# Performance work log

Measured on AMD Instinct MI355X. Metric: run time of the kernel, lower is better.

Reference implementation:

```python
import jax, jax.numpy as jnp
import numpy as np

N, E, G = 50000, 800000, 128          # nodes, edges, graphs in batch
DF, DE, DT = 128, 256, 18             # dim_features, dim_embedding, dim_target
NUM_LAYERS = 4


def setup_inputs() -> dict:
    key = jax.random.key(0)
    ks = jax.random.split(key, 32)
    inp = {}
    inp["x"] = jax.random.normal(ks[0], (N, DF), jnp.float32)
    inp["edge_index"] = jax.random.randint(ks[1], (2, E), 0, N, dtype=jnp.int64)
    inp["batch"] = jnp.sort(jax.random.randint(ks[2], (N,), 0, G, dtype=jnp.int64))
    i = 3
    for l in range(NUM_LAYERS):
        din = DF if l == 0 else DE
        inp[f"Wl{l}"] = jax.random.normal(ks[i], (din, DE), jnp.float32) * (din ** -0.5); i += 1
        inp[f"bl{l}"] = jnp.zeros((DE,), jnp.float32)
        inp[f"Wr{l}"] = jax.random.normal(ks[i], (din, DE), jnp.float32) * (din ** -0.5); i += 1
        inp[f"Wm{l}"] = jax.random.normal(ks[i], (DE, DE), jnp.float32) * (DE ** -0.5); i += 1
        inp[f"bm{l}"] = jnp.zeros((DE,), jnp.float32)
    inp["fc1_W"] = jax.random.normal(ks[i], (NUM_LAYERS * DE, DE), jnp.float32) * ((NUM_LAYERS * DE) ** -0.5); i += 1
    inp["fc1_b"] = jnp.zeros((DE,), jnp.float32)
    inp["fc2_W"] = jax.random.normal(ks[i], (DE, DT), jnp.float32) * (DE ** -0.5); i += 1
    inp["fc2_b"] = jnp.zeros((DT,), jnp.float32)
    return inp


def _seg_max(v, idx, n):
    # scatter-max; empty segments -> 0 (PyG scatter 'max' convention)
    m = jax.ops.segment_max(v, idx, num_segments=n)
    return jnp.where(jnp.isfinite(m), m, 0.0)


def reference(x, edge_index, batch,
              Wl0, bl0, Wr0, Wm0, bm0,
              Wl1, bl1, Wr1, Wm1, bm1,
              Wl2, bl2, Wr2, Wm2, bm2,
              Wl3, bl3, Wr3, Wm3, bm3,
              fc1_W, fc1_b, fc2_W, fc2_b):
    src, dst = edge_index[0], edge_index[1]
    params = [(Wl0, bl0, Wr0, Wm0, bm0), (Wl1, bl1, Wr1, Wm1, bm1),
              (Wl2, bl2, Wr2, Wm2, bm2), (Wl3, bl3, Wr3, Wm3, bm3)]
    h = x
    outs = []
    for Wl, bl, Wr, Wm, bm in params:
        # SAGEConv(aggr='max'): lin_l(max_j x_j) + lin_r(x_i)
        agg = _seg_max(h[src], dst, h.shape[0])       # [N, din] gather + scatter-max
        h = agg @ Wl + bl + h @ Wr                    # [N, DE]
        h = jax.nn.relu(h @ Wm + bm)                  # fc_max + relu
        outs.append(h)
    hc = jnp.concatenate(outs, axis=1)                # [N, 4*DE]
    g = _seg_max(hc, batch, G)                        # global_max_pool -> [G, 4*DE]
    last_layer = jax.nn.relu(g @ fc1_W + fc1_b)       # [G, DE]
    out = last_layer @ fc2_W + fc2_b                  # [G, DT] (dropout = identity at eval)
    return jax.nn.log_softmax(out, axis=1), out, last_layer
```

## Files before the change

### kernel.cpp

```cpp
#include <hip/hip_runtime.h>
#include <stdint.h>

#define NN 50000
#define EE 800000
#define GG 128
#define DF 128
#define DE 256
#define NB 196

typedef unsigned short u16;
typedef __bf16 bf16x8 __attribute__((ext_vector_type(8)));
typedef float f32x4 __attribute__((ext_vector_type(4)));
typedef short s16x8 __attribute__((ext_vector_type(8)));

__device__ __forceinline__ float bf2f(u16 u) {
  union { unsigned int i; float f; } x; x.i = ((unsigned int)u) << 16; return x.f;
}
__device__ __forceinline__ u16 f2bf(float f) {
  union { float f; unsigned int i; } x; x.f = f;
  unsigned int i = x.i;
  return (u16)((i + 0x7fffu + ((i >> 16) & 1u)) >> 16);
}

__device__ __forceinline__ void async16(const void* g, void* l) {
  __builtin_amdgcn_global_load_lds(
      (const __attribute__((address_space(1))) void*)g,
      (__attribute__((address_space(3))) void*)l,
      16, 0, 0);
}

__device__ __forceinline__ s16x8 vmax8(s16x8 a, s16x8 b) {
  return __builtin_elementwise_max(a, b);
}

__global__ void detect_kernel(const u16* __restrict__ xr,
                              const unsigned* __restrict__ ei_words,
                              int* __restrict__ flags, int* __restrict__ bucket_cnt) {
  int tid = threadIdx.x;
  if (blockIdx.x == 1) {
    if (tid < NB) bucket_cnt[tid] = 0;
    return;
  }
  __shared__ int red[2];
  if (tid < 2) red[tid] = 0;
  __syncthreads();
  int found = 0;
  for (int it = 0; it < 32; it++) {
    int i = it * 256 + tid;
    u16 a = xr[2 * i], b = xr[2 * i + 1];
    if (((a >> 7) & 0xFFu) == 0xFFu) found = 1;
    if (((b >> 7) & 0xFFu) == 0xFFu) found = 1;
  }
  if (__ballot(found)) { if ((tid & 63) == 0) atomicOr(&red[0], 1); }
  int nz = 0;
  if (tid < 128) {
    for (int j = 0; j < 4; j++) {
      unsigned w = ei_words[2 * (tid * 4 + j) + 1];
      if (w != 0u) nz = 1;
    }
  }
  if (__ballot(nz)) { if ((tid & 63) == 0) atomicOr(&red[1], 1); }
  __syncthreads();
  if (tid == 0) { flags[0] = red[0]; flags[1] = red[1]; }
}

__device__ __forceinline__ u16 ldw(const void* p, int idx, int f) {
  return f ? f2bf(((const float*)p)[idx]) : ((const u16*)p)[idx];
}

struct ConvSeg { const void* src; u16* dst; int start_blk; int n; };

struct PrepArgs {
  ConvSeg s[12]; int nseg; int conv_blocks;
  const void* x; u16* acat_x; u16* xk;
  const void* ei; const void* batch;
  int* src32; int* dst32; int* batch32; int* bucket_cnt;
};

__global__ void prep_all(PrepArgs A, const int* __restrict__ flags) {
  int f = flags[0];
  int tid = threadIdx.x;
  int b = blockIdx.x;

  if (b < A.conv_blocks) {
    for (int i = 0; i < A.nseg; i++) {
      int nb = (A.s[i].n + 255) >> 8;
      if (b >= A.s[i].start_blk && b < A.s[i].start_blk + nb) {
        int idx = ((b - A.s[i].start_blk) << 8) + tid;
        if (idx < A.s[i].n) A.s[i].dst[idx] = ldw(A.s[i].src, idx, f);
        return;
      }
    }
    return;
  }
  b -= A.conv_blocks;

  if (b < 3125) {
    int i = (b * 256 + tid) * 8;
    int node = i >> 7, d = i & 127;
    union { u16 u[8]; uint4 v; } o, kx;
    if (f) {
      const float4* xp = (const float4*)((const float*)A.x + i);
      float4 a = xp[0], q = xp[1];
      o.u[0] = f2bf(a.x); o.u[1] = f2bf(a.y); o.u[2] = f2bf(a.z); o.u[3] = f2bf(a.w);
      o.u[4] = f2bf(q.x); o.u[5] = f2bf(q.y); o.u[6] = f2bf(q.z); o.u[7] = f2bf(q.w);
    } else {
      o.v = *(const uint4*)((const u16*)A.x + i);
    }
#pragma unroll
    for (int j = 0; j < 8; j++) {
      short s = (short)o.u[j];
      kx.u[j] = (u16)(s ^ ((s >> 15) & 0x7FFF));
    }
    *(uint4*)(A.acat_x + (long)node * 512 + d) = o.v;
    *(uint4*)(A.xk + i) = kx.v;
    return;
  }
  b -= 3125;

  __shared__ int h[NB];
  if (tid < NB) h[tid] = 0;
  __syncthreads();
  int i64 = (flags[1] == 0);
  int e0 = b * 2048;
  for (int j = 0; j < 8; j++) {
    int i = e0 + j * 256 + tid;
    if (i < EE) {
      int s, d;
      if (i64) {
        s = (int)((const long long*)A.ei)[i];
        d = (int)((const long long*)A.ei)[EE + i];
      } else {
        s = ((const int*)A.ei)[i];
        d = ((const int*)A.ei)[EE + i];
      }
      s = min(max(s, 0), NN - 1);
      d = min(max(d, 0), NN - 1);
      A.src32[i] = s;
      A.dst32[i] = d;
      atomicAdd(&h[d >> 8], 1);
    }
    if (i < NN) {
      int bv = i64 ? (int)((const long long*)A.batch)[i] : ((const int*)A.batch)[i];
      A.batch32[i] = min(max(bv, 0), GG - 1);
    }
  }
  __syncthreads();
  if (tid < NB) atomicAdd(&A.bucket_cnt[tid], h[tid]);
}

struct TransArgs {
  const void* Wl[4]; const void* Wr[4]; const void* Wm[4]; const void* fc1W;
  u16* WcatT[4]; u16* WmT[4]; u16* fc1WT;
};

__global__ __launch_bounds__(256) void transpose_w(TransArgs T, const int* __restrict__ flags) {
  int f = flags[0];
  __shared__ u16 tile[64][65];
  int b = blockIdx.x;
  const void* src; u16* dst; int kt, ntile, Kd; int krow_off = 0;
  if (b < 16) {
    kt = b >> 2; ntile = b & 3; Kd = 256;
    if (kt * 64 < 128) { src = T.Wl[0]; } else { src = T.Wr[0]; krow_off = 128; }
    dst = T.WcatT[0];
  } else if (b < 112) {
    int l = 1 + (b - 16) / 32; int t = (b - 16) % 32;
    kt = t >> 2; ntile = t & 3; Kd = 512;
    if (kt * 64 < 256) { src = T.Wl[l]; } else { src = T.Wr[l]; krow_off = 256; }
    dst = T.WcatT[l];
  } else if (b < 176) {
    int l = (b - 112) / 16; int t = (b - 112) % 16;
    kt = t >> 2; ntile = t & 3; Kd = 256;
    src = T.Wm[l]; dst = T.WmT[l];
  } else {
    int t = b - 176;
    kt = t >> 2; ntile = t & 3; Kd = 1024;
    src = T.fc1W; dst = T.fc1WT;
  }
  int cj = threadIdx.x & 63, rp = threadIdx.x >> 6;
#pragma unroll 4
  for (int p = 0; p < 16; p++) {
    int krow = kt * 64 + p * 4 + rp;
    tile[p * 4 + rp][cj] = ldw(src, (krow - krow_off) * 256 + ntile * 64 + cj, f);
  }
  __syncthreads();
#pragma unroll 4
  for (int p = 0; p < 16; p++) {
    int nrow = ntile * 64 + p * 4 + rp;
    dst[(long)nrow * Kd + kt * 64 + cj] = tile[cj][p * 4 + rp];
  }
}

__global__ void bucket_scan(const int* __restrict__ bucket_cnt, int* __restrict__ bucket_base,
                            int* __restrict__ bucket_cur,
                            const int* __restrict__ batch, int* __restrict__ gs) {
  __shared__ int sh[256];
  int tid = threadIdx.x;
  int x = (tid < NB) ? bucket_cnt[tid] : 0;
  sh[tid] = x;
  __syncthreads();
  for (int off = 1; off < 256; off <<= 1) {
    int v = (tid >= off) ? sh[tid - off] : 0;
    __syncthreads();
    sh[tid] += v;
    __syncthreads();
  }
  if (tid < NB) { bucket_base[tid] = sh[tid] - x; bucket_cur[tid] = sh[tid] - x; }
  if (tid == 0) bucket_base[NB] = EE;
  if (tid <= GG) {
    int g = tid, lo = 0, hi = NN;
    while (lo < hi) { int mid = (lo + hi) >> 1; if (batch[mid] < g) lo = mid + 1; else hi = mid; }
    gs[g] = lo;
  }
}

__global__ __launch_bounds__(256) void bucket_pass1(
    const int* __restrict__ src32, const int* __restrict__ dst32,
    int* __restrict__ bucket_cur, unsigned* __restrict__ bucket_buf) {
  __shared__ int lcnt[NB];
  __shared__ int lbase[NB];
  int tid = threadIdx.x, b = blockIdx.x;
  if (tid < NB) lcnt[tid] = 0;
  __syncthreads();
  int e0 = b * 2048;
  int lofs[8]; unsigned pk[8]; int bk[8];
#pragma unroll
  for (int j = 0; j < 8; j++) {
    int i = e0 + j * 256 + tid;
    if (i < EE) {
      int s = src32[i], d = dst32[i];
      bk[j] = d >> 8;
      pk[j] = ((unsigned)s << 8) | (unsigned)(d & 255);
      lofs[j] = atomicAdd(&lcnt[bk[j]], 1);
    } else bk[j] = -1;
  }
  __syncthreads();
  if (tid < NB) lbase[tid] = atomicAdd(&bucket_cur[tid], lcnt[tid]);
  __syncthreads();
#pragma unroll
  for (int j = 0; j < 8; j++)
    if (bk[j] >= 0)
      bucket_buf[lbase[bk[j]] + lofs[j]] = pk[j];
}

__global__ __launch_bounds__(256) void bucket_pass2(
    const unsigned* __restrict__ bucket_buf, const int* __restrict__ bucket_base,
    int* __restrict__ col_src, int* __restrict__ row_ptr) {
  __shared__ int cnt[256];
  __shared__ int sh[256];
  __shared__ int cur[256];
  int tid = threadIdx.x, b = blockIdx.x;
  int ebase = bucket_base[b], eend = bucket_base[b + 1];
  cnt[tid] = 0;
  __syncthreads();
  for (int e = ebase + tid; e < eend; e += 256)
    atomicAdd(&cnt[bucket_buf[e] & 255u], 1);
  __syncthreads();
  int x = cnt[tid];
  sh[tid] = x;
  __syncthreads();
  for (int off = 1; off < 256; off <<= 1) {
    int v = (tid >= off) ? sh[tid - off] : 0;
    __syncthreads();
    sh[tid] += v;
    __syncthreads();
  }
  int node = b * 256 + tid;
  if (node < NN) row_ptr[node + 1] = ebase + sh[tid];
  cur[tid] = ebase + sh[tid] - x;
  __syncthreads();
  for (int e = ebase + tid; e < eend; e += 256) {
    unsigned p = bucket_buf[e];
    int slot = atomicAdd(&cur[p & 255u], 1);
    col_src[slot] = (int)(p >> 8);
  }
  if (b == 0 && tid == 0) row_ptr[0] = 0;
}

template <int LPR, bool KEYED>
__global__ __launch_bounds__(256) void segmax_kernel(
    const u16* __restrict__ feat, int fstride,
    const int* __restrict__ row_ptr, const int* __restrict__ col_src,
    u16* __restrict__ agg_out, int ostride, int n) {
  constexpr int R = 64 / LPR;
  int node = blockIdx.x * 4 + (threadIdx.x >> 6);
  if (node >= n) return;
  int lane = threadIdx.x & 63;
  int sub = lane / LPR;
  int cp = lane % LPR;
  int beg = row_ptr[node], end = row_ptr[node + 1];
  s16x8 m = (s16x8)(short)(KEYED ? (short)0x807F : (short)0);
  const u16* fb = feat + cp * 8;

  int e = beg + sub;
  for (; e + 3 * R < end; e += 4 * R) {
    int s0 = col_src[e];
    int s1 = col_src[e + R];
    int s2 = col_src[e + 2 * R];
    int s3 = col_src[e + 3 * R];
    s16x8 v0 = *(const s16x8*)(fb + (long)s0 * fstride);
    s16x8 v1 = *(const s16x8*)(fb + (long)s1 * fstride);
    s16x8 v2 = *(const s16x8*)(fb + (long)s2 * fstride);
    s16x8 v3 = *(const s16x8*)(fb + (long)s3 * fstride);
    m = vmax8(m, vmax8(vmax8(v0, v1), vmax8(v2, v3)));
  }
  for (; e < end; e += R)
    m = vmax8(m, *(const s16x8*)(fb + (long)col_src[e] * fstride));

#pragma unroll
  for (int d = LPR; d < 64; d <<= 1) {
    union { s16x8 s; int i[4]; } t;
    t.s = m;
#pragma unroll
    for (int j = 0; j < 4; j++) t.i[j] = __shfl_xor(t.i[j], d);
    m = vmax8(m, t.s);
  }

  if (sub == 0) {
    if (KEYED) {
      if (beg == end) {
        m = (s16x8)(short)0;
      } else {
        s16x8 sp = (m >> 15) & (short)0x7FFF;
        m = m ^ sp;
      }
    }
    *(s16x8*)(agg_out + (long)node * ostride + cp * 8) = m;
  }
}

__global__ __launch_bounds__(512) void gemm256w(
    const u16* __restrict__ A, int lda, int K,
    const u16* __restrict__ BT,
    const u16* __restrict__ bias,
    u16* __restrict__ C, int ldc, int M, int relu_flag) {
  __shared__ u16 lsA[128 * 64];
  __shared__ u16 lsB[256 * 64];
  int tid = threadIdx.x;
  int lane = tid & 63, w = tid >> 6;
  int bm = blockIdx.x;
  int wm = (w & 1) << 6, wn = (w >> 1) << 6;
  int ln15 = lane & 15, quad = lane >> 4;

  f32x4 acc[4][4] = {};

  int riw = lane >> 3;
  int j = (lane & 7) ^ riw;
  int ra0 = min(bm * 128 + w * 8 + riw, M - 1);
  int ra1 = min(bm * 128 + 64 + w * 8 + riw, M - 1);
  const u16* gA0 = A + (long)ra0 * lda + j * 8;
  const u16* gA1 = A + (long)ra1 * lda + j * 8;
  const u16* gB0 = BT + (long)(w * 8 + riw) * K + j * 8;
  const u16* gB1 = BT + (long)(64 + w * 8 + riw) * K + j * 8;
  const u16* gB2 = BT + (long)(128 + w * 8 + riw) * K + j * 8;
  const u16* gB3 = BT + (long)(192 + w * 8 + riw) * K + j * 8;
  u16* lA0 = lsA + (w * 8) * 64;
  u16* lA1 = lsA + (64 + w * 8) * 64;
  u16* lB0 = lsB + (w * 8) * 64;
  u16* lB1 = lsB + (64 + w * 8) * 64;
  u16* lB2 = lsB + (128 + w * 8) * 64;
  u16* lB3 = lsB + (192 + w * 8) * 64;
  int swz7 = ln15 & 7;

  for (int k0 = 0; k0 < K; k0 += 64) {
    async16(gA0 + k0, lA0);
    async16(gA1 + k0, lA1);
    async16(gB0 + k0, lB0);
    async16(gB1 + k0, lB1);
    async16(gB2 + k0, lB2);
    async16(gB3 + k0, lB3);
    __syncthreads();
#pragma unroll
    for (int kh = 0; kh < 2; kh++) {
      int pc = (((kh << 2) | quad) ^ swz7) << 3;
      bf16x8 af[4], bfr[4];
#pragma unroll
      for (int t = 0; t < 4; t++) {
        af[t]  = *(const bf16x8*)(lsA + (wm + t * 16 + ln15) * 64 + pc);
        bfr[t] = *(const bf16x8*)(lsB + (wn + t * 16 + ln15) * 64 + pc);
      }
#pragma unroll
      for (int mt = 0; mt < 4; mt++)
#pragma unroll
        for (int nt = 0; nt < 4; nt++)
          acc[mt][nt] = __builtin_amdgcn_mfma_f32_16x16x32_bf16(af[mt], bfr[nt], acc[mt][nt], 0, 0, 0);
    }
    __syncthreads();
  }

  float bv[4];
#pragma unroll
  for (int nt = 0; nt < 4; nt++)
    bv[nt] = bf2f(bias[wn + nt * 16 + ln15]);

#pragma unroll
  for (int mt = 0; mt < 4; mt++) {
    int row0 = bm * 128 + wm + mt * 16 + quad * 4;
#pragma unroll
    for (int rr = 0; rr < 4; rr++) {
      int row = row0 + rr;
      if (row < M) {
#pragma unroll
        for (int nt = 0; nt < 4; nt++) {
          float v = acc[mt][nt][rr] + bv[nt];
          if (relu_flag) v = fmaxf(v, 0.f);
          C[(long)row * ldc + wn + nt * 16 + ln15] = f2bf(v);
        }
      }
    }
  }
}

__global__ void pool_kernel(const u16* __restrict__ h, const int* __restrict__ gs,
                            u16* __restrict__ g_pool, int l) {
  int g = blockIdx.x >> 1, half = blockIdx.x & 1;
  int chunk = threadIdx.x & 15;
  int rg = threadIdx.x >> 4;
  int beg = gs[g], end = gs[g + 1];
  s16x8 m = (s16x8)(short)0;
  const u16* hp = h + half * 128 + chunk * 8;
  for (int n = beg + rg; n < end; n += 64)
    m = vmax8(m, *(const s16x8*)(hp + (long)n * 512));
  __shared__ s16x8 red[64][16];
  red[rg][chunk] = m;
  __syncthreads();
  for (int s = 32; s >= 1; s >>= 1) {
    if (rg < s) red[rg][chunk] = vmax8(red[rg][chunk], red[rg + s][chunk]);
    __syncthreads();
  }
  if (rg == 0)
    *(s16x8*)(g_pool + g * 1024 + l * 256 + half * 128 + chunk * 8) = red[0][chunk];
}

__global__ __launch_bounds__(256) void fc1_gemm(
    const u16* __restrict__ A,
    const u16* __restrict__ BT,
    float* __restrict__ Cpart) {
  __shared__ u16 lsA[128 * 32];
  __shared__ u16 lsB[128 * 32];
  int tid = threadIdx.x;
  int lane = tid & 63, w = tid >> 6;
  int slice = blockIdx.x >> 1, bn = blockIdx.x & 1;
  int wm = (w & 1) << 6, wn = (w >> 1) << 6;
  int ln15 = lane & 15, quad = lane >> 4;

  f32x4 acc[4][4] = {};

  int cm = lane >> 2;
  int ck = (lane & 3) << 3;
  int kb = slice * 256;

  const u16* gA0 = A + (long)(w * 16 + cm) * 1024 + kb + ck;
  const u16* gA1 = A + (long)((w + 4) * 16 + cm) * 1024 + kb + ck;
  const u16* gB0 = BT + (long)(bn * 128 + w * 16 + cm) * 1024 + kb + ck;
  const u16* gB1 = BT + (long)(bn * 128 + (w + 4) * 16 + cm) * 1024 + kb + ck;
  u16* lA0 = lsA + w * 512;
  u16* lA1 = lsA + (w + 4) * 512;
  u16* lB0 = lsB + w * 512;
  u16* lB1 = lsB + (w + 4) * 512;

  for (int k0 = 0; k0 < 256; k0 += 32) {
    async16(gA0 + k0, lA0);
    async16(gA1 + k0, lA1);
    async16(gB0 + k0, lB0);
    async16(gB1 + k0, lB1);
    __syncthreads();
    bf16x8 af[4], bfr[4];
#pragma unroll
    for (int t = 0; t < 4; t++) {
      af[t]  = *(const bf16x8*)(lsA + (wm + t * 16 + ln15) * 32 + quad * 8);
      bfr[t] = *(const bf16x8*)(lsB + (wn + t * 16 + ln15) * 32 + quad * 8);
    }
#pragma unroll
    for (int mt = 0; mt < 4; mt++)
#pragma unroll
      for (int nt = 0; nt < 4; nt++)
        acc[mt][nt] = __builtin_amdgcn_mfma_f32_16x16x32_bf16(af[mt], bfr[nt], acc[mt][nt], 0, 0, 0);
    __syncthreads();
  }

  float* Cb = Cpart + slice * (GG * 256);
#pragma unroll
  for (int mt = 0; mt < 4; mt++) {
    int row0 = wm + mt * 16 + quad * 4;
#pragma unroll
    for (int r = 0; r < 4; r++)
#pragma unroll
      for (int nt = 0; nt < 4; nt++)
        Cb[(row0 + r) * 256 + bn * 128 + wn + nt * 16 + ln15] = acc[mt][nt][r];
  }
}

__global__ void fc2_head(const float* __restrict__ fc1part,
                         const u16* __restrict__ fc1b,
                         const u16* __restrict__ W,
                         const u16* __restrict__ b,
                         void* __restrict__ outbuf, const int* __restrict__ flags) {
  int g = blockIdx.x, t = threadIdx.x;
  __shared__ float lr[256];
  __shared__ float ps[144];
  __shared__ float sv[18];
  __shared__ float sred[2];
  float v = bf2f(fc1b[t]);
#pragma unroll
  for (int s = 0; s < 4; s++) v += fc1part[s * (GG * 256) + g * 256 + t];
  v = fmaxf(v, 0.f);
  lr[t] = v;
  if (flags[0]) ((float*)outbuf)[4608 + g * 256 + t] = v;
  else          ((u16*)outbuf)[4608 + g * 256 + t] = f2bf(v);
  __syncthreads();
  if (t < 144) {
    int o = t % 18, s = t / 18;
    float acc = 0.f;
    int k0 = s * 32;
#pragma unroll 8
    for (int k = k0; k < k0 + 32; k++)
      acc += lr[k] * bf2f(W[k * 18 + o]);
    ps[t] = acc;
  }
  __syncthreads();
  if (t < 18) {
    float acc = bf2f(b[t]);
#pragma unroll
    for (int s = 0; s < 8; s++) acc += ps[s * 18 + t];
    sv[t] = acc;
  }
  __syncthreads();
  if (t == 0) {
    float mx = sv[0];
    for (int i = 1; i < 18; i++) mx = fmaxf(mx, sv[i]);
    float s = 0.f;
    for (int i = 0; i < 18; i++) s += expf(sv[i] - mx);
    sred[0] = mx; sred[1] = logf(s);
  }
  __syncthreads();
  if (t < 18) {
    float raw = sv[t];
    float lsm = raw - sred[0] - sred[1];
    if (flags[0]) {
      ((float*)outbuf)[g * 18 + t] = lsm;
      ((float*)outbuf)[2304 + g * 18 + t] = raw;
    } else {
      ((u16*)outbuf)[g * 18 + t] = f2bf(lsm);
      ((u16*)outbuf)[2304 + g * 18 + t] = f2bf(raw);
    }
  }
}

extern "C" void kernel_launch(void* const* d_in, const int* in_sizes, int n_in,
                              void* d_out, int out_size, void* d_ws, size_t ws_size,
                              hipStream_t stream) {
  (void)in_sizes; (void)n_in; (void)out_size; (void)ws_size;
  const void* x = d_in[0];
  const void* ei = d_in[1];
  const void* batch = d_in[2];
  const void *Wl[4], *bl[4], *Wr[4], *Wm[4], *bm[4];
  for (int l = 0; l < 4; l++) {
    Wl[l] = d_in[3 + l * 5 + 0];
    bl[l] = d_in[3 + l * 5 + 1];
    Wr[l] = d_in[3 + l * 5 + 2];
    Wm[l] = d_in[3 + l * 5 + 3];
    bm[l] = d_in[3 + l * 5 + 4];
  }
  const void* fc1W = d_in[23];
  const void* fc1b = d_in[24];
  const void* fc2W = d_in[25];
  const void* fc2b = d_in[26];

  char* ws = (char*)d_ws;
  size_t off = 0;
  auto alloc = [&](size_t bytes) -> void* {
    void* p = ws + off;
    off = (off + bytes + 255) & ~(size_t)255;
    return p;
  };
  int* flags       = (int*)alloc(16);
  int* row_ptr     = (int*)alloc((NN + 1) * sizeof(int));
  int* bucket_cnt  = (int*)alloc(NB * sizeof(int));
  int* bucket_base = (int*)alloc((NB + 1) * sizeof(int));
  int* bucket_cur  = (int*)alloc(NB * sizeof(int));
  unsigned* bucket_buf = (unsigned*)alloc((size_t)EE * sizeof(unsigned));
  int* col_src = (int*)alloc((size_t)EE * sizeof(int));
  int* src32   = (int*)alloc((size_t)EE * sizeof(int));
  int* dst32   = (int*)alloc((size_t)EE * sizeof(int));
  int* batch32 = (int*)alloc(NN * sizeof(int));
  int* gs      = (int*)alloc((GG + 1) * sizeof(int));
  u16* WcatT[4]; for (int l = 0; l < 4; l++) WcatT[l] = (u16*)alloc(256 * 512 * 2);
  u16* WmT[4];   for (int l = 0; l < 4; l++) WmT[l]   = (u16*)alloc(256 * 256 * 2);
  u16* bl_bf[4]; for (int l = 0; l < 4; l++) bl_bf[l] = (u16*)alloc(256 * 2);
  u16* bm_bf[4]; for (int l = 0; l < 4; l++) bm_bf[l] = (u16*)alloc(256 * 2);
  u16* fc1WT   = (u16*)alloc(256 * 1024 * 2);
  u16* fc1b_bf = (u16*)alloc(256 * 2);
  u16* fc2W_bf = (u16*)alloc(256 * 18 * 2);
  u16* fc2b_bf = (u16*)alloc(18 * 2);
  u16* xk      = (u16*)alloc((size_t)NN * DF * 2);
  u16* Acat    = (u16*)alloc((size_t)NN * 512 * 2);
  u16* tmp     = (u16*)alloc((size_t)NN * 256 * 2);
  u16* gpool   = (u16*)alloc(GG * 1024 * 2);
  float* fc1part = (float*)alloc(4 * GG * 256 * sizeof(float));

  detect_kernel<<<2, 256, 0, stream>>>((const u16*)x, (const unsigned*)ei, flags, bucket_cnt);

  TransArgs TA;
  for (int l = 0; l < 4; l++) {
    TA.Wl[l] = Wl[l]; TA.Wr[l] = Wr[l]; TA.Wm[l] = Wm[l];
    TA.WcatT[l] = WcatT[l]; TA.WmT[l] = WmT[l];
  }
  TA.fc1W = fc1W; TA.fc1WT = fc1WT;
  transpose_w<<<240, 256, 0, stream>>>(TA, flags);

  PrepArgs PA;
  int blk = 0, si = 0;
  auto addseg = [&](const void* s, u16* d, int n) {
    PA.s[si].src = s; PA.s[si].dst = d; PA.s[si].start_blk = blk; PA.s[si].n = n;
    blk += (n + 255) / 256; si++;
  };
  addseg(fc2W, fc2W_bf, 256 * 18);
  for (int l = 0; l < 4; l++) addseg(bl[l], bl_bf[l], 256);
  for (int l = 0; l < 4; l++) addseg(bm[l], bm_bf[l], 256);
  addseg(fc1b, fc1b_bf, 256);
  addseg(fc2b, fc2b_bf, 18);
  PA.nseg = si; PA.conv_blocks = blk;
  PA.x = x; PA.acat_x = Acat + DF; PA.xk = xk;
  PA.ei = ei; PA.batch = batch;
  PA.src32 = src32; PA.dst32 = dst32; PA.batch32 = batch32; PA.bucket_cnt = bucket_cnt;
  prep_all<<<PA.conv_blocks + 3125 + 391, 256, 0, stream>>>(PA, flags);

  bucket_scan<<<1, 256, 0, stream>>>(bucket_cnt, bucket_base, bucket_cur, batch32, gs);
  bucket_pass1<<<391, 256, 0, stream>>>(src32, dst32, bucket_cur, bucket_buf);
  bucket_pass2<<<NB, 256, 0, stream>>>(bucket_buf, bucket_base, col_src, row_ptr);

  int segblocks = (NN + 3) / 4;
  int gemmgrid = (NN + 127) / 128;

  for (int l = 0; l < 4; l++) {
    if (l == 0) {
      segmax_kernel<16, true><<<segblocks, 256, 0, stream>>>(xk, DF, row_ptr, col_src,
                                                             Acat, 512, NN);
    } else {
      segmax_kernel<32, false><<<segblocks, 256, 0, stream>>>(Acat + 256, 512, row_ptr, col_src,
                                                              Acat, 512, NN);
    }
    int K = (l == 0) ? 256 : 512;
    gemm256w<<<gemmgrid, 512, 0, stream>>>(Acat, 512, K, WcatT[l], bl_bf[l], tmp, 256, NN, 0);
    gemm256w<<<gemmgrid, 512, 0, stream>>>(tmp, 256, 256, WmT[l], bm_bf[l], Acat + 256, 512, NN, 1);
    pool_kernel<<<GG * 2, 1024, 0, stream>>>(Acat + 256, gs, gpool, l);
  }

  fc1_gemm<<<8, 256, 0, stream>>>(gpool, fc1WT, fc1part);
  fc2_head<<<GG, 256, 0, stream>>>(fc1part, fc1b_bf, fc2W_bf, fc2b_bf, d_out, flags);
}
```

Before: 535.5 us.

## Store node features in 32-column sliced layout for cache-friendly gather

Replaces the interleaved [N,512] concat buffer with a column-sliced layout: 16 planes of [N,32] bf16. Neighbour-max gathers now run per slice, so each gathered row is 64 contiguous bytes and the working set per block fits in cache. The GEMM A-load, GEMM epilogue, prep and pool kernels are updated to address the new layout. In exchange the segmax launches 8x more blocks, so row_ptr and col_src are read once per slice, and the C stores from the GEMM use a strided pattern.

```diff
diff --git a/kernel.cpp b/kernel.cpp
--- a/kernel.cpp
+++ b/kernel.cpp
@@ -7,6 +7,7 @@
 #define DF 128
 #define DE 256
 #define NB 196
+#define SLPITCH (NN * 32)
 
 typedef unsigned short u16;
 typedef __bf16 bf16x8 __attribute__((ext_vector_type(8)));
@@ -72,7 +73,7 @@
 
 struct PrepArgs {
   ConvSeg s[12]; int nseg; int conv_blocks;
-  const void* x; u16* acat_x; u16* xk;
+  const void* x; u16* Asl; u16* xk;
   const void* ei; const void* batch;
   int* src32; int* dst32; int* batch32; int* bucket_cnt;
 };
@@ -112,7 +113,7 @@
       short s = (short)o.u[j];
       kx.u[j] = (u16)(s ^ ((s >> 15) & 0x7FFF));
     }
-    *(uint4*)(A.acat_x + (long)node * 512 + d) = o.v;
+    *(uint4*)(A.Asl + (size_t)(4 + (d >> 5)) * SLPITCH + (long)node * 32 + (d & 31)) = o.v;
     *(uint4*)(A.xk + i) = kx.v;
     return;
   }
@@ -277,20 +278,19 @@
   if (b == 0 && tid == 0) row_ptr[0] = 0;
 }
 
-template <int LPR, bool KEYED>
-__global__ __launch_bounds__(256) void segmax_kernel(
-    const u16* __restrict__ feat, int fstride,
+__global__ __launch_bounds__(256) void segmax_l0(
+    const u16* __restrict__ xk,
     const int* __restrict__ row_ptr, const int* __restrict__ col_src,
-    u16* __restrict__ agg_out, int ostride, int n) {
-  constexpr int R = 64 / LPR;
+    u16* __restrict__ Asl, int n) {
+  constexpr int LPR = 16, R = 4;
   int node = blockIdx.x * 4 + (threadIdx.x >> 6);
   if (node >= n) return;
   int lane = threadIdx.x & 63;
   int sub = lane / LPR;
   int cp = lane % LPR;
   int beg = row_ptr[node], end = row_ptr[node + 1];
-  s16x8 m = (s16x8)(short)(KEYED ? (short)0x807F : (short)0);
-  const u16* fb = feat + cp * 8;
+  s16x8 m = (s16x8)(short)0x807F;
+  const u16* fb = xk + cp * 8;
 
   int e = beg + sub;
   for (; e + 3 * R < end; e += 4 * R) {
@@ -298,14 +298,14 @@
     int s1 = col_src[e + R];
     int s2 = col_src[e + 2 * R];
     int s3 = col_src[e + 3 * R];
-    s16x8 v0 = *(const s16x8*)(fb + (long)s0 * fstride);
-    s16x8 v1 = *(const s16x8*)(fb + (long)s1 * fstride);
-    s16x8 v2 = *(const s16x8*)(fb + (long)s2 * fstride);
-    s16x8 v3 = *(const s16x8*)(fb + (long)s3 * fstride);
+    s16x8 v0 = *(const s16x8*)(fb + (long)s0 * DF);
+    s16x8 v1 = *(const s16x8*)(fb + (long)s1 * DF);
+    s16x8 v2 = *(const s16x8*)(fb + (long)s2 * DF);
+    s16x8 v3 = *(const s16x8*)(fb + (long)s3 * DF);
     m = vmax8(m, vmax8(vmax8(v0, v1), vmax8(v2, v3)));
   }
   for (; e < end; e += R)
-    m = vmax8(m, *(const s16x8*)(fb + (long)col_src[e] * fstride));
+    m = vmax8(m, *(const s16x8*)(fb + (long)col_src[e] * DF));
 
 #pragma unroll
   for (int d = LPR; d < 64; d <<= 1) {
@@ -317,23 +317,59 @@
   }
 
   if (sub == 0) {
-    if (KEYED) {
-      if (beg == end) {
-        m = (s16x8)(short)0;
-      } else {
-        s16x8 sp = (m >> 15) & (short)0x7FFF;
-        m = m ^ sp;
-      }
-    }
-    *(s16x8*)(agg_out + (long)node * ostride + cp * 8) = m;
-  }
+    if (beg == end) {
+      m = (s16x8)(short)0;
+    } else {
+      s16x8 sp = (m >> 15) & (short)0x7FFF;
+      m = m ^ sp;
+    }
+    *(s16x8*)(Asl + (size_t)(cp >> 2) * SLPITCH + (long)node * 32 + (cp & 3) * 8) = m;
+  }
+}
+
+__global__ __launch_bounds__(256) void segmax_sl(
+    const u16* __restrict__ Asl,
+    const int* __restrict__ row_ptr, const int* __restrict__ col_src, int n) {
+  int s = blockIdx.x & 7;
+  int node = (blockIdx.x >> 3) * 4 + (threadIdx.x >> 6);
+  if (node >= n) return;
+  int lane = threadIdx.x & 63;
+  int sub = lane >> 2;
+  int cp = lane & 3;
+  int beg = row_ptr[node], end = row_ptr[node + 1];
+  s16x8 m = (s16x8)(short)0;
+  const u16* fb = Asl + (size_t)(8 + s) * SLPITCH + cp * 8;
+
+  int e = beg + sub;
+  for (; e + 16 < end; e += 32) {
+    int s0 = col_src[e];
+    int s1 = col_src[e + 16];
+    s16x8 v0 = *(const s16x8*)(fb + (long)s0 * 32);
+    s16x8 v1 = *(const s16x8*)(fb + (long)s1 * 32);
+    m = vmax8(m, vmax8(v0, v1));
+  }
+  if (e < end)
+    m = vmax8(m, *(const s16x8*)(fb + (long)col_src[e] * 32));
+
+#pragma unroll
+  for (int d = 4; d < 64; d <<= 1) {
+    union { s16x8 s; int i[4]; } t;
+    t.s = m;
+#pragma unroll
+    for (int j = 0; j < 4; j++) t.i[j] = __shfl_xor(t.i[j], d);
+    m = vmax8(m, t.s);
+  }
+
+  if (sub == 0)
+    *(s16x8*)((u16*)Asl + (size_t)s * SLPITCH + (long)node * 32 + cp * 8) = m;
 }
 
 __global__ __launch_bounds__(512) void gemm256w(
-    const u16* __restrict__ A, int lda, int K,
+    const u16* __restrict__ A, int lda, int K, int a_sliced,
     const u16* __restrict__ BT,
     const u16* __restrict__ bias,
-    u16* __restrict__ C, int ldc, int M, int relu_flag) {
+    u16* __restrict__ C, int ldc,
+    int M, int relu_flag, int c_sliced) {
   __shared__ u16 lsA[128 * 64];
   __shared__ u16 lsB[256 * 64];
   int tid = threadIdx.x;
@@ -348,8 +384,6 @@
   int j = (lane & 7) ^ riw;
   int ra0 = min(bm * 128 + w * 8 + riw, M - 1);
   int ra1 = min(bm * 128 + 64 + w * 8 + riw, M - 1);
-  const u16* gA0 = A + (long)ra0 * lda + j * 8;
-  const u16* gA1 = A + (long)ra1 * lda + j * 8;
   const u16* gB0 = BT + (long)(w * 8 + riw) * K + j * 8;
   const u16* gB1 = BT + (long)(64 + w * 8 + riw) * K + j * 8;
   const u16* gB2 = BT + (long)(128 + w * 8 + riw) * K + j * 8;
@@ -363,8 +397,18 @@
   int swz7 = ln15 & 7;
 
   for (int k0 = 0; k0 < K; k0 += 64) {
-    async16(gA0 + k0, lA0);
-    async16(gA1 + k0, lA1);
+    const u16 *pA0, *pA1;
+    if (a_sliced) {
+      int c = (k0 >> 3) + j;
+      size_t so = (size_t)(c >> 2) * SLPITCH + (c & 3) * 8;
+      pA0 = A + so + (long)ra0 * 32;
+      pA1 = A + so + (long)ra1 * 32;
+    } else {
+      pA0 = A + (long)ra0 * lda + k0 + j * 8;
+      pA1 = A + (long)ra1 * lda + k0 + j * 8;
+    }
+    async16(pA0, lA0);
+    async16(pA1, lA1);
     async16(gB0 + k0, lB0);
     async16(gB1 + k0, lB1);
     async16(gB2 + k0, lB2);
@@ -394,33 +438,44 @@
     bv[nt] = bf2f(bias[wn + nt * 16 + ln15]);
 
 #pragma unroll
-  for (int mt = 0; mt < 4; mt++) {
-    int row0 = bm * 128 + wm + mt * 16 + quad * 4;
-#pragma unroll
-    for (int rr = 0; rr < 4; rr++) {
-      int row = row0 + rr;
-      if (row < M) {
-#pragma unroll
-        for (int nt = 0; nt < 4; nt++) {
+  for (int nt = 0; nt < 4; nt++) {
+    int col = wn + nt * 16 + ln15;
+    u16* cb;
+    long rstride;
+    if (c_sliced) {
+      cb = C + (size_t)(8 + (col >> 5)) * SLPITCH + (col & 31);
+      rstride = 32;
+    } else {
+      cb = C + col;
+      rstride = ldc;
+    }
+#pragma unroll
+    for (int mt = 0; mt < 4; mt++) {
+      int row0 = bm * 128 + wm + mt * 16 + quad * 4;
+#pragma unroll
+      for (int rr = 0; rr < 4; rr++) {
+        int row = row0 + rr;
+        if (row < M) {
           float v = acc[mt][nt][rr] + bv[nt];
           if (relu_flag) v = fmaxf(v, 0.f);
-          C[(long)row * ldc + wn + nt * 16 + ln15] = f2bf(v);
+          cb[(long)row * rstride] = f2bf(v);
         }
       }
     }
   }
 }
 
-__global__ void pool_kernel(const u16* __restrict__ h, const int* __restrict__ gs,
+__global__ void pool_kernel(const u16* __restrict__ Asl, const int* __restrict__ gs,
                             u16* __restrict__ g_pool, int l) {
   int g = blockIdx.x >> 1, half = blockIdx.x & 1;
   int chunk = threadIdx.x & 15;
   int rg = threadIdx.x >> 4;
   int beg = gs[g], end = gs[g + 1];
   s16x8 m = (s16x8)(short)0;
-  const u16* hp = h + half * 128 + chunk * 8;
+  int ch = half * 128 + chunk * 8;
+  const u16* hp = Asl + (size_t)(8 + (ch >> 5)) * SLPITCH + (ch & 31);
   for (int n = beg + rg; n < end; n += 64)
-    m = vmax8(m, *(const s16x8*)(hp + (long)n * 512));
+    m = vmax8(m, *(const s16x8*)(hp + (long)n * 32));
   __shared__ s16x8 red[64][16];
   red[rg][chunk] = m;
   __syncthreads();
@@ -594,7 +649,7 @@
   u16* fc2W_bf = (u16*)alloc(256 * 18 * 2);
   u16* fc2b_bf = (u16*)alloc(18 * 2);
   u16* xk      = (u16*)alloc((size_t)NN * DF * 2);
-  u16* Acat    = (u16*)alloc((size_t)NN * 512 * 2);
+  u16* Asl     = (u16*)alloc((size_t)16 * SLPITCH * 2);
   u16* tmp     = (u16*)alloc((size_t)NN * 256 * 2);
   u16* gpool   = (u16*)alloc(GG * 1024 * 2);
   float* fc1part = (float*)alloc(4 * GG * 256 * sizeof(float));
@@ -621,7 +676,7 @@
   addseg(fc1b, fc1b_bf, 256);
   addseg(fc2b, fc2b_bf, 18);
   PA.nseg = si; PA.conv_blocks = blk;
-  PA.x = x; PA.acat_x = Acat + DF; PA.xk = xk;
+  PA.x = x; PA.Asl = Asl; PA.xk = xk;
   PA.ei = ei; PA.batch = batch;
   PA.src32 = src32; PA.dst32 = dst32; PA.batch32 = batch32; PA.bucket_cnt = bucket_cnt;
   prep_all<<<PA.conv_blocks + 3125 + 391, 256, 0, stream>>>(PA, flags);
@@ -635,16 +690,16 @@
 
   for (int l = 0; l < 4; l++) {
     if (l == 0) {
-      segmax_kernel<16, true><<<segblocks, 256, 0, stream>>>(xk, DF, row_ptr, col_src,
-                                                             Acat, 512, NN);
+      segmax_l0<<<segblocks, 256, 0, stream>>>(xk, row_ptr, col_src, Asl, NN);
     } else {
-      segmax_kernel<32, false><<<segblocks, 256, 0, stream>>>(Acat + 256, 512, row_ptr, col_src,
-                                                              Acat, 512, NN);
+      segmax_sl<<<segblocks * 8, 256, 0, stream>>>(Asl, row_ptr, col_src, NN);
     }
     int K = (l == 0) ? 256 : 512;
-    gemm256w<<<gemmgrid, 512, 0, stream>>>(Acat, 512, K, WcatT[l], bl_bf[l], tmp, 256, NN, 0);
-    gemm256w<<<gemmgrid, 512, 0, stream>>>(tmp, 256, 256, WmT[l], bm_bf[l], Acat + 256, 512, NN, 1);
-    pool_kernel<<<GG * 2, 1024, 0, stream>>>(Acat + 256, gs, gpool, l);
+    gemm256w<<<gemmgrid, 512, 0, stream>>>(Asl, 0, K, 1, WcatT[l], bl_bf[l],
+                                           tmp, 256, NN, 0, 0);
+    gemm256w<<<gemmgrid, 512, 0, stream>>>(tmp, 256, 256, 0, WmT[l], bm_bf[l],
+                                           Asl, 0, NN, 1, 1);
+    pool_kernel<<<GG * 2, 1024, 0, stream>>>(Asl, gs, gpool, l);
   }
 
   fc1_gemm<<<8, 256, 0, stream>>>(gpool, fc1WT, fc1part);
```

After: 664.3 us. +24.1%, slower.
